# Kernel optimization log

Measured on AMD Instinct MI355X. Metric: run time of the kernel, lower is better.

Reference implementation:

```python
import jax, jax.numpy as jnp
import numpy as np

H = 1024      # hidden_size
NH = 16       # num_heads
HD = H // NH  # head_dim
BETA = 1.0
STEPS = 2
EPS_NORM = 1e-12  # F.normalize eps
EPS_LN = 1e-5     # LayerNorm eps


def setup_inputs() -> dict:
    key = jax.random.key(0)
    ks = jax.random.split(key, 10)
    s = 1.0 / np.sqrt(H)
    return {
        "hidden_states": jax.random.normal(ks[0], (2, 2048, H), jnp.float32),
        "Wq": jax.random.normal(ks[1], (H, H), jnp.float32) * s,
        "bq": jnp.zeros((H,), jnp.float32),
        "Wk": jax.random.normal(ks[2], (H, H), jnp.float32) * s,
        "bk": jnp.zeros((H,), jnp.float32),
        "Wv": jax.random.normal(ks[3], (H, H), jnp.float32) * s,
        "bv": jnp.zeros((H,), jnp.float32),
        "Wo": jax.random.normal(ks[4], (H, H), jnp.float32) * s,
        "bo": jnp.zeros((H,), jnp.float32),
        "ln_w": jnp.ones((H,), jnp.float32),
        "ln_b": jnp.zeros((H,), jnp.float32),
    }


def _l2norm(x):
    n = jnp.linalg.norm(x, axis=-1, keepdims=True)
    return x / jnp.maximum(n, EPS_NORM)


def reference(hidden_states, Wq, bq, Wk, bk, Wv, bv, Wo, bo, ln_w, ln_b):
    B, S, _ = hidden_states.shape
    residual = hidden_states
    # LayerNorm
    mu = jnp.mean(hidden_states, axis=-1, keepdims=True)
    var = jnp.mean(jnp.square(hidden_states - mu), axis=-1, keepdims=True)
    x = (hidden_states - mu) * jax.lax.rsqrt(var + EPS_LN) * ln_w + ln_b
    # projections -> [B,S,NH,HD]
    q = (x @ Wq + bq).reshape(B, S, NH, HD)
    k = (x @ Wk + bk).reshape(B, S, NH, HD)
    v = (x @ Wv + bv).reshape(B, S, NH, HD)
    # cosine-normalized Hopfield retrieval (normalization only once, before loop)
    q = _l2norm(q)
    k = _l2norm(k)
    state = q
    for _ in range(STEPS):
        sim = jnp.einsum('bqhd,bkhd->bqhk', state, k)
        att = jax.nn.softmax(BETA * sim, axis=-1)
        state = jnp.einsum('bqhk,bkhd->bqhd', att, v)
    o = state.reshape(B, S, H) @ Wo + bo
    return residual + o
```

## Files before the change

kernel.cpp:

```cpp
#include <hip/hip_runtime.h>
#include <hip/hip_bf16.h>
#include <math.h>

#define HDIM 1024
#define NHEADS 16
#define HEADD 64
#define SEQLEN 2048
#define NBATCH 2
#define NROWS (NBATCH*SEQLEN)
#define NBH (NBATCH*NHEADS)
#define LOG2E 1.44269504f
#define NT 32

typedef float f32x4 __attribute__((ext_vector_type(4)));
typedef float f32x16 __attribute__((ext_vector_type(16)));
typedef short short8 __attribute__((ext_vector_type(8)));
typedef unsigned short us4v __attribute__((ext_vector_type(4)));

#define GLOBAL_AS __attribute__((address_space(1)))
#define LDS_AS __attribute__((address_space(3)))

union F4 { float4 v; float f[4]; };
union PW { unsigned int u[4]; short8 s; };

static __device__ __forceinline__ unsigned short f2bf(float x) {
    __hip_bfloat16 h = __float2bfloat16(x);
    return *(unsigned short*)&h;
}

__global__ __launch_bounds__(256) void ln_kernel(
        const float* __restrict__ x, const float* __restrict__ w,
        const float* __restrict__ b, unsigned short* __restrict__ xn) {
    int row = blockIdx.x;
    F4 vv; vv.v = ((const float4*)(x + (size_t)row*HDIM))[threadIdx.x];
    float s  = vv.f[0]+vv.f[1]+vv.f[2]+vv.f[3];
    float ss = vv.f[0]*vv.f[0]+vv.f[1]*vv.f[1]+vv.f[2]*vv.f[2]+vv.f[3]*vv.f[3];
    #pragma unroll
    for (int off = 32; off > 0; off >>= 1) {
        s  += __shfl_xor(s, off);
        ss += __shfl_xor(ss, off);
    }
    __shared__ float red[8];
    int wid = threadIdx.x >> 6;
    if ((threadIdx.x & 63) == 0) { red[wid] = s; red[wid+4] = ss; }
    __syncthreads();
    s  = red[0]+red[1]+red[2]+red[3];
    ss = red[4]+red[5]+red[6]+red[7];
    float mean = s * (1.0f/HDIM);
    float var  = ss * (1.0f/HDIM) - mean*mean;
    float rstd = rsqrtf(var + 1e-5f);
    F4 wv; wv.v = ((const float4*)w)[threadIdx.x];
    F4 bv; bv.v = ((const float4*)b)[threadIdx.x];
    us4v o;
    #pragma unroll
    for (int j = 0; j < 4; ++j)
        o[j] = f2bf((vv.f[j]-mean)*rstd*wv.f[j] + bv.f[j]);
    *(us4v*)(xn + (size_t)row*HDIM + threadIdx.x*4) = o;
}

__global__ __launch_bounds__(256) void wconv_kernel(
        const float* __restrict__ W0, const float* __restrict__ W1,
        const float* __restrict__ W2, const float* __restrict__ W3,
        unsigned short* __restrict__ WtBase) {
    __shared__ unsigned short T[64*72];
    int z = blockIdx.z;
    const float* W = (z == 0) ? W0 : (z == 1) ? W1 : (z == 2) ? W2 : W3;
    unsigned short* Wt = WtBase + (size_t)z*HDIM*HDIM;
    int k0 = blockIdx.x*64, n0 = blockIdx.y*64;
    int t = threadIdx.x;
    #pragma unroll
    for (int it = 0; it < 4; ++it) {
        int r = (t>>4) + it*16;
        int c = (t&15)*4;
        F4 x; x.v = *(const float4*)(W + (size_t)(k0+r)*HDIM + n0 + c);
        #pragma unroll
        for (int j = 0; j < 4; ++j) T[(c+j)*72 + r] = f2bf(x.f[j]);
    }
    __syncthreads();
    #pragma unroll
    for (int it = 0; it < 2; ++it) {
        int n = (t>>3) + it*32;
        int ch = t&7;
        short8 rowv = *(const short8*)(T + n*72 + ch*8);
        *(short8*)(Wt + (size_t)(n0+n)*HDIM + k0 + ch*8) = rowv;
    }
}

__global__ __launch_bounds__(256) void gemm_qkv_kernel(
        const unsigned short* __restrict__ A,
        const unsigned short* __restrict__ WtBase,
        const float* __restrict__ bq, const float* __restrict__ bk,
        const float* __restrict__ bv,
        unsigned short* __restrict__ qb, unsigned short* __restrict__ kb,
        unsigned short* __restrict__ vt) {
    __shared__ unsigned short As[2][128*64];
    __shared__ unsigned short Bs[2][128*64];
    int m0 = blockIdx.x * 128;
    int yy = blockIdx.y;
    int mat = yy >> 3;
    int n0 = (yy & 7) * 128;
    const unsigned short* Wt = WtBase + (size_t)mat*HDIM*HDIM;
    const float* bias = (mat == 0) ? bq : (mat == 1) ? bk : bv;
    int t = threadIdx.x;
    int wid = t >> 6, l = t & 63;
    int wm = wid >> 1, wn = wid & 1;
    int lq = l & 15, g = l >> 4;
    f32x4 acc[4][4];
    #pragma unroll
    for (int mi = 0; mi < 4; ++mi)
        #pragma unroll
        for (int ni = 0; ni < 4; ++ni) acc[mi][ni] = 0.0f;

    auto STAGE = [&](int b, int k0) {
        #pragma unroll
        for (int i = 0; i < 4; ++i) {
            int idx = t + 256*i;
            int r = idx >> 3, ch = idx & 7;
            int gch = ch ^ (r & 7);
            __builtin_amdgcn_global_load_lds(
                (const GLOBAL_AS void*)(A + (size_t)(m0+r)*HDIM + k0 + gch*8),
                (LDS_AS void*)((char*)&As[b][0] + idx*16), 16, 0, 0);
            __builtin_amdgcn_global_load_lds(
                (const GLOBAL_AS void*)(Wt + (size_t)(n0+r)*HDIM + k0 + gch*8),
                (LDS_AS void*)((char*)&Bs[b][0] + idx*16), 16, 0, 0);
        }
    };

    STAGE(0, 0);
    asm volatile("s_waitcnt vmcnt(0)" ::: "memory");
    __builtin_amdgcn_s_barrier();
    asm volatile("" ::: "memory");
    int buf = 0;
    for (int ks = 0; ks < 16; ++ks) {
        if (ks < 15) STAGE(buf^1, (ks+1)*64);
        const char* Ab = (const char*)&As[buf][0];
        const char* Bb = (const char*)&Bs[buf][0];
        #pragma unroll
        for (int kc = 0; kc < 2; ++kc) {
            short8 af[4], bf[4];
            #pragma unroll
            for (int mi = 0; mi < 4; ++mi) {
                int r = wm*64 + mi*16 + lq;
                af[mi] = *(const short8*)(Ab + r*128 + (((kc*4+g) ^ (r&7))<<4));
            }
            #pragma unroll
            for (int ni = 0; ni < 4; ++ni) {
                int r = wn*64 + ni*16 + lq;
                bf[ni] = *(const short8*)(Bb + r*128 + (((kc*4+g) ^ (r&7))<<4));
            }
            #pragma unroll
            for (int mi = 0; mi < 4; ++mi)
                #pragma unroll
                for (int ni = 0; ni < 4; ++ni)
                    acc[mi][ni] = __builtin_amdgcn_mfma_f32_16x16x32_bf16(
                        af[mi], bf[ni], acc[mi][ni], 0, 0, 0);
        }
        asm volatile("s_waitcnt vmcnt(0)" ::: "memory");
        __builtin_amdgcn_s_barrier();
        asm volatile("" ::: "memory");
        buf ^= 1;
    }
    float bvv[4];
    #pragma unroll
    for (int ni = 0; ni < 4; ++ni) bvv[ni] = bias[n0 + wn*64 + ni*16 + lq];
    #pragma unroll
    for (int mi = 0; mi < 4; ++mi)
        #pragma unroll
        for (int ni = 0; ni < 4; ++ni)
            #pragma unroll
            for (int i = 0; i < 4; ++i) acc[mi][ni][i] += bvv[ni];
    int h = (n0 >> 6) + wn;
    if (mat <= 1) {
        unsigned short* outp = (mat == 0) ? qb : kb;
        float oscale = (mat == 0) ? LOG2E : 1.0f;
        #pragma unroll
        for (int mi = 0; mi < 4; ++mi) {
            f32x4 ss = 0.0f;
            #pragma unroll
            for (int ni = 0; ni < 4; ++ni)
                #pragma unroll
                for (int i = 0; i < 4; ++i) ss[i] += acc[mi][ni][i]*acc[mi][ni][i];
            #pragma unroll
            for (int off = 1; off < 16; off <<= 1)
                #pragma unroll
                for (int i = 0; i < 4; ++i) ss[i] += __shfl_xor(ss[i], off);
            #pragma unroll
            for (int i = 0; i < 4; ++i) {
                float sc = oscale / fmaxf(sqrtf(ss[i]), 1e-12f);
                int m = m0 + wm*64 + mi*16 + g*4 + i;
                int bb = m >> 11, sq = m & (SEQLEN-1);
                unsigned short* orow = outp
                    + ((size_t)(bb*NHEADS + h)*SEQLEN + sq)*HEADD;
                #pragma unroll
                for (int ni = 0; ni < 4; ++ni)
                    orow[ni*16 + lq] = f2bf(acc[mi][ni][i] * sc);
            }
        }
    } else {
        #pragma unroll
        for (int mi = 0; mi < 4; ++mi) {
            int m = m0 + wm*64 + mi*16 + g*4;
            int bb = m >> 11, sq = m & (SEQLEN-1);
            #pragma unroll
            for (int ni = 0; ni < 4; ++ni) {
                int d = ni*16 + lq;
                us4v pk;
                #pragma unroll
                for (int i = 0; i < 4; ++i) pk[i] = f2bf(acc[mi][ni][i]);
                *(us4v*)(vt + ((size_t)(bb*NHEADS + h)*HEADD + d)*SEQLEN + sq) = pk;
            }
        }
    }
}

__global__ __launch_bounds__(256) void gemm_o_kernel(
        const unsigned short* __restrict__ A,
        const unsigned short* __restrict__ Wt,
        const float* __restrict__ bias,
        const float* __restrict__ residual,
        float* __restrict__ out) {
    __shared__ unsigned short As[2][128*64];
    __shared__ unsigned short Bs[2][64*64];
    int m0 = blockIdx.x * 128;
    int n0 = blockIdx.y * 64;
    int t = threadIdx.x;
    int wid = t >> 6, l = t & 63;
    int wm = wid >> 1, wn = wid & 1;
    int lq = l & 15, g = l >> 4;
    f32x4 acc[4][2];
    #pragma unroll
    for (int mi = 0; mi < 4; ++mi)
        #pragma unroll
        for (int ni = 0; ni < 2; ++ni) acc[mi][ni] = 0.0f;

    auto STAGE = [&](int b, int k0) {
        #pragma unroll
        for (int i = 0; i < 4; ++i) {
            int idx = t + 256*i;
            int r = idx >> 3, ch = idx & 7;
            int gch = ch ^ (r & 7);
            __builtin_amdgcn_global_load_lds(
                (const GLOBAL_AS void*)(A + (size_t)(m0+r)*HDIM + k0 + gch*8),
                (LDS_AS void*)((char*)&As[b][0] + idx*16), 16, 0, 0);
        }
        #pragma unroll
        for (int i = 0; i < 2; ++i) {
            int idx = t + 256*i;
            int r = idx >> 3, ch = idx & 7;
            int gch = ch ^ (r & 7);
            __builtin_amdgcn_global_load_lds(
                (const GLOBAL_AS void*)(Wt + (size_t)(n0+r)*HDIM + k0 + gch*8),
                (LDS_AS void*)((char*)&Bs[b][0] + idx*16), 16, 0, 0);
        }
    };

    STAGE(0, 0);
    asm volatile("s_waitcnt vmcnt(0)" ::: "memory");
    __builtin_amdgcn_s_barrier();
    asm volatile("" ::: "memory");
    int buf = 0;
    for (int ks = 0; ks < 16; ++ks) {
        if (ks < 15) STAGE(buf^1, (ks+1)*64);
        const char* Ab = (const char*)&As[buf][0];
        const char* Bb = (const char*)&Bs[buf][0];
        #pragma unroll
        for (int kc = 0; kc < 2; ++kc) {
            short8 af[4], bf[2];
            #pragma unroll
            for (int mi = 0; mi < 4; ++mi) {
                int r = wm*64 + mi*16 + lq;
                af[mi] = *(const short8*)(Ab + r*128 + (((kc*4+g) ^ (r&7))<<4));
            }
            #pragma unroll
            for (int ni = 0; ni < 2; ++ni) {
                int r = wn*32 + ni*16 + lq;
                bf[ni] = *(const short8*)(Bb + r*128 + (((kc*4+g) ^ (r&7))<<4));
            }
            #pragma unroll
            for (int mi = 0; mi < 4; ++mi)
                #pragma unroll
                for (int ni = 0; ni < 2; ++ni)
                    acc[mi][ni] = __builtin_amdgcn_mfma_f32_16x16x32_bf16(
                        af[mi], bf[ni], acc[mi][ni], 0, 0, 0);
        }
        asm volatile("s_waitcnt vmcnt(0)" ::: "memory");
        __builtin_amdgcn_s_barrier();
        asm volatile("" ::: "memory");
        buf ^= 1;
    }
    float bvv[2];
    #pragma unroll
    for (int ni = 0; ni < 2; ++ni) bvv[ni] = bias[n0 + wn*32 + ni*16 + lq];
    #pragma unroll
    for (int mi = 0; mi < 4; ++mi)
        #pragma unroll
        for (int i = 0; i < 4; ++i) {
            int m = m0 + wm*64 + mi*16 + g*4 + i;
            float* orow = out + (size_t)m*HDIM;
            const float* rrow = residual + (size_t)m*HDIM;
            #pragma unroll
            for (int ni = 0; ni < 2; ++ni) {
                int n = n0 + wn*32 + ni*16 + lq;
                orow[n] = acc[mi][ni][i] + bvv[ni] + rrow[n];
            }
        }
}

__global__ __launch_bounds__(512, 4) void attn_fused_kernel(
        const unsigned short* __restrict__ qg, const unsigned short* __restrict__ kg,
        const unsigned short* __restrict__ vtg, unsigned short* __restrict__ outp) {
    __shared__ char L[4*16384];
    int b = blockIdx.x;
    int bh = (b & 7)*4 + ((b >> 3) & 3);
    int q0 = (b >> 5) * 128;
    int t = threadIdx.x;
    int wid = t >> 6, l = t & 63;
    int wq = wid >> 1, ks = wid & 1;
    int q = l & 31, hi = l >> 5, r7 = q & 7;
    short8 qf[4];
    {
        const unsigned short* qrow = qg + ((size_t)bh*SEQLEN + q0 + wq*32 + q)*HEADD;
        #pragma unroll
        for (int dc = 0; dc < 4; ++dc) qf[dc] = *(const short8*)(qrow + dc*16 + hi*8);
    }
    int koffv[4];
    #pragma unroll
    for (int x = 0; x < 4; ++x) koffv[x] = q*128 + (((x*2 + hi) ^ r7) << 4);
    int vofA = koffv[2*ks], vofB = koffv[2*ks+1];

    f32x16 o0 = 0.0f, o1 = 0.0f;
    float ls = 0.0f;
    const unsigned short* Kg = kg + (size_t)bh*SEQLEN*HEADD;
    const unsigned short* Vg = vtg + (size_t)bh*HEADD*SEQLEN;
    unsigned int* slot = (unsigned int*)(L + wq*4096);
    float* slsum = (float*)(L + 16384 + wq*256);

    int sr = t >> 3, sch = t & 7;
    int sgch = sch ^ (sr & 7);
    const unsigned short* Ksrc = Kg + sr*HEADD + sgch*8;
    const unsigned short* Vsrc = Vg + (size_t)sr*SEQLEN + sgch*8;
    auto STAGE = [&](int buf, int kt) {
        __builtin_amdgcn_global_load_lds(
            (const GLOBAL_AS void*)(Ksrc + (size_t)kt*4096),
            (LDS_AS void*)(L + buf*16384 + t*16), 16, 0, 0);
        __builtin_amdgcn_global_load_lds(
            (const GLOBAL_AS void*)(Vsrc + kt*64),
            (LDS_AS void*)(L + buf*16384 + 8192 + t*16), 16, 0, 0);
    };

    auto doTile = [&](const char* KL, const char* VL) {
        short8 kf0 = *(const short8*)(KL + koffv[0]);
        short8 kf1 = *(const short8*)(KL + koffv[1]);
        short8 kf2 = *(const short8*)(KL + koffv[2]);
        short8 kf3 = *(const short8*)(KL + koffv[3]);
        f32x16 s = 0.0f;
        __builtin_amdgcn_s_setprio(1);
        s = __builtin_amdgcn_mfma_f32_32x32x16_bf16(kf0, qf[0], s, 0, 0, 0);
        s = __builtin_amdgcn_mfma_f32_32x32x16_bf16(kf1, qf[1], s, 0, 0, 0);
        s = __builtin_amdgcn_mfma_f32_32x32x16_bf16(kf2, qf[2], s, 0, 0, 0);
        s = __builtin_amdgcn_mfma_f32_32x32x16_bf16(kf3, qf[3], s, 0, 0, 0);
        __builtin_amdgcn_s_setprio(0);
        unsigned int w[8];
        #pragma unroll
        for (int i = 0; i < 8; ++i) {
            float e0 = __builtin_amdgcn_exp2f(s[2*i]);
            float e1 = __builtin_amdgcn_exp2f(s[2*i+1]);
            ls += e0 + e1;
            asm("v_cvt_pk_bf16_f32 %0, %1, %2" : "=v"(w[i]) : "v"(e0), "v"(e1));
        }
        asm volatile("v_permlane32_swap_b32 %0, %1" : "+v"(w[0]), "+v"(w[2]));
        asm volatile("v_permlane32_swap_b32 %0, %1" : "+v"(w[1]), "+v"(w[3]));
        asm volatile("v_permlane32_swap_b32 %0, %1" : "+v"(w[4]), "+v"(w[6]));
        asm volatile("v_permlane32_swap_b32 %0, %1" : "+v"(w[5]), "+v"(w[7]));
        PW pa, pb;
        pa.u[0]=w[0]; pa.u[1]=w[1]; pa.u[2]=w[2]; pa.u[3]=w[3];
        pb.u[0]=w[4]; pb.u[1]=w[5]; pb.u[2]=w[6]; pb.u[3]=w[7];
        short8 va0 = *(const short8*)(VL + vofA);
        short8 va1 = *(const short8*)(VL + vofA + 4096);
        short8 vb0 = *(const short8*)(VL + vofB);
        short8 vb1 = *(const short8*)(VL + vofB + 4096);
        __builtin_amdgcn_s_setprio(1);
        o0 = __builtin_amdgcn_mfma_f32_32x32x16_bf16(va0, pa.s, o0, 0, 0, 0);
        o1 = __builtin_amdgcn_mfma_f32_32x32x16_bf16(va1, pa.s, o1, 0, 0, 0);
        o0 = __builtin_amdgcn_mfma_f32_32x32x16_bf16(vb0, pb.s, o0, 0, 0, 0);
        o1 = __builtin_amdgcn_mfma_f32_32x32x16_bf16(vb1, pb.s, o1, 0, 0, 0);
        __builtin_amdgcn_s_setprio(0);
    };

    auto runPass = [&]() {
        for (int p = 0; p < NT/2; ++p) {
            int ba = (p & 1) * 2;
            if (p < NT/2 - 1) { STAGE(ba^2, 2*p+2); STAGE((ba^2)+1, 2*p+3); }
            doTile(L + ba*16384 + ks*4096, L + ba*16384 + 8192);
            doTile(L + (ba+1)*16384 + ks*4096, L + (ba+1)*16384 + 8192);
            asm volatile("s_waitcnt vmcnt(0)" ::: "memory");
            __builtin_amdgcn_s_barrier();
            asm volatile("" ::: "memory");
        }
    };

    STAGE(0, 0); STAGE(1, 1);
    asm volatile("s_waitcnt vmcnt(0)" ::: "memory");
    __builtin_amdgcn_s_barrier();
    asm volatile("" ::: "memory");
    runPass();
    ls += __shfl_xor(ls, 32);
    if (ks == 1) {
        #pragma unroll
        for (int i = 0; i < 8; ++i) {
            unsigned int u;
            asm("v_cvt_pk_bf16_f32 %0, %1, %2" : "=v"(u) : "v"(o0[2*i]), "v"(o0[2*i+1]));
            slot[i*64 + l] = u;
            asm("v_cvt_pk_bf16_f32 %0, %1, %2" : "=v"(u) : "v"(o1[2*i]), "v"(o1[2*i+1]));
            slot[(8+i)*64 + l] = u;
        }
        slsum[l] = ls;
        asm volatile("s_waitcnt lgkmcnt(0)" ::: "memory");
    }
    __builtin_amdgcn_s_barrier();
    asm volatile("" ::: "memory");
    if (ks == 0) {
        #pragma unroll
        for (int i = 0; i < 8; ++i) {
            unsigned int u = slot[i*64 + l];
            o0[2*i]   += __uint_as_float(u << 16);
            o0[2*i+1] += __uint_as_float(u & 0xffff0000u);
            u = slot[(8+i)*64 + l];
            o1[2*i]   += __uint_as_float(u << 16);
            o1[2*i+1] += __uint_as_float(u & 0xffff0000u);
        }
        float osc = LOG2E / (ls + slsum[l]);
        unsigned int w0[8], w1[8];
        #pragma unroll
        for (int i = 0; i < 8; ++i) {
            float a0 = o0[2*i]*osc, a1 = o0[2*i+1]*osc;
            asm("v_cvt_pk_bf16_f32 %0, %1, %2" : "=v"(w0[i]) : "v"(a0), "v"(a1));
            float b0 = o1[2*i]*osc, b1 = o1[2*i+1]*osc;
            asm("v_cvt_pk_bf16_f32 %0, %1, %2" : "=v"(w1[i]) : "v"(b0), "v"(b1));
        }
        asm volatile("v_permlane32_swap_b32 %0, %1" : "+v"(w0[0]), "+v"(w0[2]));
        asm volatile("v_permlane32_swap_b32 %0, %1" : "+v"(w0[1]), "+v"(w0[3]));
        asm volatile("v_permlane32_swap_b32 %0, %1" : "+v"(w0[4]), "+v"(w0[6]));
        asm volatile("v_permlane32_swap_b32 %0, %1" : "+v"(w0[5]), "+v"(w0[7]));
        asm volatile("v_permlane32_swap_b32 %0, %1" : "+v"(w1[0]), "+v"(w1[2]));
        asm volatile("v_permlane32_swap_b32 %0, %1" : "+v"(w1[1]), "+v"(w1[3]));
        asm volatile("v_permlane32_swap_b32 %0, %1" : "+v"(w1[4]), "+v"(w1[6]));
        asm volatile("v_permlane32_swap_b32 %0, %1" : "+v"(w1[5]), "+v"(w1[7]));
        PW pa;
        pa.u[0]=w0[0]; pa.u[1]=w0[1]; pa.u[2]=w0[2]; pa.u[3]=w0[3]; qf[0]=pa.s;
        pa.u[0]=w0[4]; pa.u[1]=w0[5]; pa.u[2]=w0[6]; pa.u[3]=w0[7]; qf[1]=pa.s;
        pa.u[0]=w1[0]; pa.u[1]=w1[1]; pa.u[2]=w1[2]; pa.u[3]=w1[3]; qf[2]=pa.s;
        pa.u[0]=w1[4]; pa.u[1]=w1[5]; pa.u[2]=w1[6]; pa.u[3]=w1[7]; qf[3]=pa.s;
        #pragma unroll
        for (int i = 0; i < 8; ++i) {
            slot[i*64 + l] = w0[i];
            slot[(8+i)*64 + l] = w1[i];
        }
        asm volatile("s_waitcnt lgkmcnt(0)" ::: "memory");
    }
    __builtin_amdgcn_s_barrier();
    asm volatile("" ::: "memory");
    if (ks == 1) {
        PW pa;
        pa.u[0]=slot[0*64+l]; pa.u[1]=slot[1*64+l]; pa.u[2]=slot[2*64+l]; pa.u[3]=slot[3*64+l]; qf[0]=pa.s;
        pa.u[0]=slot[4*64+l]; pa.u[1]=slot[5*64+l]; pa.u[2]=slot[6*64+l]; pa.u[3]=slot[7*64+l]; qf[1]=pa.s;
        pa.u[0]=slot[8*64+l]; pa.u[1]=slot[9*64+l]; pa.u[2]=slot[10*64+l]; pa.u[3]=slot[11*64+l]; qf[2]=pa.s;
        pa.u[0]=slot[12*64+l]; pa.u[1]=slot[13*64+l]; pa.u[2]=slot[14*64+l]; pa.u[3]=slot[15*64+l]; qf[3]=pa.s;
    }
    asm volatile("s_waitcnt lgkmcnt(0)" ::: "memory");
    __builtin_amdgcn_s_barrier();
    asm volatile("" ::: "memory");
    o0 = 0.0f; o1 = 0.0f; ls = 0.0f;
    STAGE(0, 0); STAGE(1, 1);
    asm volatile("s_waitcnt vmcnt(0)" ::: "memory");
    __builtin_amdgcn_s_barrier();
    asm volatile("" ::: "memory");
    runPass();
    ls += __shfl_xor(ls, 32);
    if (ks == 1) {
        #pragma unroll
        for (int i = 0; i < 8; ++i) {
            unsigned int u;
            asm("v_cvt_pk_bf16_f32 %0, %1, %2" : "=v"(u) : "v"(o0[2*i]), "v"(o0[2*i+1]));
            slot[i*64 + l] = u;
            asm("v_cvt_pk_bf16_f32 %0, %1, %2" : "=v"(u) : "v"(o1[2*i]), "v"(o1[2*i+1]));
            slot[(8+i)*64 + l] = u;
        }
        slsum[l] = ls;
        asm volatile("s_waitcnt lgkmcnt(0)" ::: "memory");
    }
    __builtin_amdgcn_s_barrier();
    asm volatile("" ::: "memory");
    if (ks == 0) {
        #pragma unroll
        for (int i = 0; i < 8; ++i) {
            unsigned int u = slot[i*64 + l];
            o0[2*i]   += __uint_as_float(u << 16);
            o0[2*i+1] += __uint_as_float(u & 0xffff0000u);
            u = slot[(8+i)*64 + l];
            o1[2*i]   += __uint_as_float(u << 16);
            o1[2*i+1] += __uint_as_float(u & 0xffff0000u);
        }
        float osc = 1.0f / (ls + slsum[l]);
        int bb = bh >> 4, hh = bh & 15;
        unsigned short* orow = outp + ((size_t)bb*SEQLEN + q0 + wq*32 + q)*HDIM + hh*HEADD;
        const int dtab[8] = {0,2,8,10,16,18,24,26};
        #pragma unroll
        for (int i = 0; i < 8; ++i) {
            int d = dtab[i] + 4*hi;
            unsigned int wv;
            float a0 = o0[2*i]*osc, a1 = o0[2*i+1]*osc;
            asm("v_cvt_pk_bf16_f32 %0, %1, %2" : "=v"(wv) : "v"(a0), "v"(a1));
            *(unsigned int*)(orow + d) = wv;
            float c0 = o1[2*i]*osc, c1 = o1[2*i+1]*osc;
            asm("v_cvt_pk_bf16_f32 %0, %1, %2" : "=v"(wv) : "v"(c0), "v"(c1));
            *(unsigned int*)(orow + 32 + d) = wv;
        }
    }
}

extern "C" void kernel_launch(void* const* d_in, const int* in_sizes, int n_in,
                              void* d_out, int out_size, void* d_ws, size_t ws_size,
                              hipStream_t stream) {
    const float* hs = (const float*)d_in[0];
    const float* Wq = (const float*)d_in[1];
    const float* bq = (const float*)d_in[2];
    const float* Wk = (const float*)d_in[3];
    const float* bk = (const float*)d_in[4];
    const float* Wv = (const float*)d_in[5];
    const float* bv = (const float*)d_in[6];
    const float* Wo = (const float*)d_in[7];
    const float* bo = (const float*)d_in[8];
    const float* lw = (const float*)d_in[9];
    const float* lb = (const float*)d_in[10];
    unsigned short* ws16 = (unsigned short*)d_ws;
    const size_t NE = (size_t)NROWS * HDIM;
    const size_t WE = (size_t)HDIM * HDIM;
    unsigned short* xn  = ws16;
    unsigned short* Wtq = xn + NE;
    unsigned short* Wto = Wtq + 3*WE;
    unsigned short* qb  = Wtq + 4*WE;
    unsigned short* kb  = qb + NE;
    unsigned short* vt  = kb + NE;
    unsigned short* s2  = vt + NE;

    ln_kernel<<<NROWS, 256, 0, stream>>>(hs, lw, lb, xn);
    wconv_kernel<<<dim3(HDIM/64, HDIM/64, 4), 256, 0, stream>>>(Wq, Wk, Wv, Wo, Wtq);
    gemm_qkv_kernel<<<dim3(NROWS/128, 24), 256, 0, stream>>>(xn, Wtq, bq, bk, bv, qb, kb, vt);
    attn_fused_kernel<<<NBH*16, 512, 0, stream>>>(qb, kb, vt, s2);
    gemm_o_kernel<<<dim3(NROWS/128, HDIM/64), 256, 0, stream>>>(s2, Wto, bo, hs, (float*)d_out);
}
```

Before: 168.7 us.

## Switch attention K/V staging to a 3-buffer ring with per-tile partial waits

Replaces the pair-wise double buffering of 64-key tiles (four 16KB LDS buffers) with a triple-buffered ring (three buffers). It prefetches two tiles ahead, processes one tile per iteration, and waits with vmcnt(2) so the newest prefetch stays in flight across the barrier. The V fragment loads are hoisted to just after the QK MFMAs, with sched_barriers pinning the order. The aim is to overlap global loads with compute more continuously and to use less LDS, which may allow more blocks per CU. The cost is twice as many barriers per pass and ordering constraints that depend on exact vmcnt accounting.

Result: faster. 160.1 us (-5.1%).

```diff
diff --git a/kernel.cpp b/kernel.cpp
--- a/kernel.cpp
+++ b/kernel.cpp
@@ -309,7 +309,7 @@
 __global__ __launch_bounds__(512, 4) void attn_fused_kernel(
         const unsigned short* __restrict__ qg, const unsigned short* __restrict__ kg,
         const unsigned short* __restrict__ vtg, unsigned short* __restrict__ outp) {
-    __shared__ char L[4*16384];
+    __shared__ char L[3*16384];
     int b = blockIdx.x;
     int bh = (b & 7)*4 + ((b >> 3) & 3);
     int q0 = (b >> 5) * 128;
@@ -323,10 +323,12 @@
         #pragma unroll
         for (int dc = 0; dc < 4; ++dc) qf[dc] = *(const short8*)(qrow + dc*16 + hi*8);
     }
-    int koffv[4];
-    #pragma unroll
-    for (int x = 0; x < 4; ++x) koffv[x] = q*128 + (((x*2 + hi) ^ r7) << 4);
-    int vofA = koffv[2*ks], vofB = koffv[2*ks+1];
+    int koffK0 = q*128 + (((0 + hi) ^ r7) << 4) + ks*4096;
+    int koffK1 = q*128 + (((2 + hi) ^ r7) << 4) + ks*4096;
+    int koffK2 = q*128 + (((4 + hi) ^ r7) << 4) + ks*4096;
+    int koffK3 = q*128 + (((6 + hi) ^ r7) << 4) + ks*4096;
+    int vofA = q*128 + (((4*ks + hi) ^ r7) << 4);
+    int vofB = q*128 + (((4*ks + 2 + hi) ^ r7) << 4);
 
     f32x16 o0 = 0.0f, o1 = 0.0f;
     float ls = 0.0f;
@@ -348,61 +350,75 @@
             (LDS_AS void*)(L + buf*16384 + 8192 + t*16), 16, 0, 0);
     };
 
-    auto doTile = [&](const char* KL, const char* VL) {
-        short8 kf0 = *(const short8*)(KL + koffv[0]);
-        short8 kf1 = *(const short8*)(KL + koffv[1]);
-        short8 kf2 = *(const short8*)(KL + koffv[2]);
-        short8 kf3 = *(const short8*)(KL + koffv[3]);
+    auto doTile = [&](const char* T) {
+        short8 k0 = *(const short8*)(T + koffK0);
+        short8 k1 = *(const short8*)(T + koffK1);
+        short8 k2 = *(const short8*)(T + koffK2);
+        short8 k3 = *(const short8*)(T + koffK3);
         f32x16 s = 0.0f;
-        __builtin_amdgcn_s_setprio(1);
-        s = __builtin_amdgcn_mfma_f32_32x32x16_bf16(kf0, qf[0], s, 0, 0, 0);
-        s = __builtin_amdgcn_mfma_f32_32x32x16_bf16(kf1, qf[1], s, 0, 0, 0);
-        s = __builtin_amdgcn_mfma_f32_32x32x16_bf16(kf2, qf[2], s, 0, 0, 0);
-        s = __builtin_amdgcn_mfma_f32_32x32x16_bf16(kf3, qf[3], s, 0, 0, 0);
-        __builtin_amdgcn_s_setprio(0);
+        s = __builtin_amdgcn_mfma_f32_32x32x16_bf16(k0, qf[0], s, 0, 0, 0);
+        s = __builtin_amdgcn_mfma_f32_32x32x16_bf16(k1, qf[1], s, 0, 0, 0);
+        s = __builtin_amdgcn_mfma_f32_32x32x16_bf16(k2, qf[2], s, 0, 0, 0);
+        s = __builtin_amdgcn_mfma_f32_32x32x16_bf16(k3, qf[3], s, 0, 0, 0);
+        __builtin_amdgcn_sched_barrier(0);
+        short8 va0 = *(const short8*)(T + 8192 + vofA);
+        short8 va1 = *(const short8*)(T + 8192 + vofA + 4096);
+        short8 vb0 = *(const short8*)(T + 8192 + vofB);
+        short8 vb1 = *(const short8*)(T + 8192 + vofB + 4096);
         unsigned int w[8];
+        float p = 0.0f;
         #pragma unroll
         for (int i = 0; i < 8; ++i) {
             float e0 = __builtin_amdgcn_exp2f(s[2*i]);
             float e1 = __builtin_amdgcn_exp2f(s[2*i+1]);
-            ls += e0 + e1;
+            p += e0 + e1;
             asm("v_cvt_pk_bf16_f32 %0, %1, %2" : "=v"(w[i]) : "v"(e0), "v"(e1));
         }
-        asm volatile("v_permlane32_swap_b32 %0, %1" : "+v"(w[0]), "+v"(w[2]));
-        asm volatile("v_permlane32_swap_b32 %0, %1" : "+v"(w[1]), "+v"(w[3]));
-        asm volatile("v_permlane32_swap_b32 %0, %1" : "+v"(w[4]), "+v"(w[6]));
-        asm volatile("v_permlane32_swap_b32 %0, %1" : "+v"(w[5]), "+v"(w[7]));
-        PW pa, pb;
-        pa.u[0]=w[0]; pa.u[1]=w[1]; pa.u[2]=w[2]; pa.u[3]=w[3];
-        pb.u[0]=w[4]; pb.u[1]=w[5]; pb.u[2]=w[6]; pb.u[3]=w[7];
-        short8 va0 = *(const short8*)(VL + vofA);
-        short8 va1 = *(const short8*)(VL + vofA + 4096);
-        short8 vb0 = *(const short8*)(VL + vofB);
-        short8 vb1 = *(const short8*)(VL + vofB + 4096);
-        __builtin_amdgcn_s_setprio(1);
-        o0 = __builtin_amdgcn_mfma_f32_32x32x16_bf16(va0, pa.s, o0, 0, 0, 0);
-        o1 = __builtin_amdgcn_mfma_f32_32x32x16_bf16(va1, pa.s, o1, 0, 0, 0);
-        o0 = __builtin_amdgcn_mfma_f32_32x32x16_bf16(vb0, pb.s, o0, 0, 0, 0);
-        o1 = __builtin_amdgcn_mfma_f32_32x32x16_bf16(vb1, pb.s, o1, 0, 0, 0);
-        __builtin_amdgcn_s_setprio(0);
+        ls += p;
+        asm("v_permlane32_swap_b32 %0, %1" : "+v"(w[0]), "+v"(w[2]));
+        asm("v_permlane32_swap_b32 %0, %1" : "+v"(w[1]), "+v"(w[3]));
+        asm("v_permlane32_swap_b32 %0, %1" : "+v"(w[4]), "+v"(w[6]));
+        asm("v_permlane32_swap_b32 %0, %1" : "+v"(w[5]), "+v"(w[7]));
+        __builtin_amdgcn_sched_barrier(0);
+        {
+            PW pa, pb;
+            pa.u[0]=w[0]; pa.u[1]=w[1]; pa.u[2]=w[2]; pa.u[3]=w[3];
+            pb.u[0]=w[4]; pb.u[1]=w[5]; pb.u[2]=w[6]; pb.u[3]=w[7];
+            __builtin_amdgcn_s_setprio(1);
+            o0 = __builtin_amdgcn_mfma_f32_32x32x16_bf16(va0, pa.s, o0, 0, 0, 0);
+            o1 = __builtin_amdgcn_mfma_f32_32x32x16_bf16(va1, pa.s, o1, 0, 0, 0);
+            o0 = __builtin_amdgcn_mfma_f32_32x32x16_bf16(vb0, pb.s, o0, 0, 0, 0);
+            o1 = __builtin_amdgcn_mfma_f32_32x32x16_bf16(vb1, pb.s, o1, 0, 0, 0);
+            __builtin_amdgcn_s_setprio(0);
+        }
     };
 
     auto runPass = [&]() {
-        for (int p = 0; p < NT/2; ++p) {
-            int ba = (p & 1) * 2;
-            if (p < NT/2 - 1) { STAGE(ba^2, 2*p+2); STAGE((ba^2)+1, 2*p+3); }
-            doTile(L + ba*16384 + ks*4096, L + ba*16384 + 8192);
-            doTile(L + (ba+1)*16384 + ks*4096, L + (ba+1)*16384 + 8192);
-            asm volatile("s_waitcnt vmcnt(0)" ::: "memory");
+        int cur = 0;
+        #pragma unroll 1
+        for (int kt = 0; kt < NT; ++kt) {
+            bool pre = (kt + 2 < NT);
+            if (pre) {
+                int nb = cur + 2; if (nb >= 3) nb -= 3;
+                STAGE(nb, kt + 2);
+            }
+            doTile(L + cur*16384);
+            if (pre) asm volatile("s_waitcnt vmcnt(2)" ::: "memory");
+            else     asm volatile("s_waitcnt vmcnt(0)" ::: "memory");
             __builtin_amdgcn_s_barrier();
             asm volatile("" ::: "memory");
+            cur = (cur == 2) ? 0 : cur + 1;
         }
     };
 
-    STAGE(0, 0); STAGE(1, 1);
-    asm volatile("s_waitcnt vmcnt(0)" ::: "memory");
-    __builtin_amdgcn_s_barrier();
-    asm volatile("" ::: "memory");
+    auto prologue = [&]() {
+        STAGE(0, 0); STAGE(1, 1);
+        asm volatile("s_waitcnt vmcnt(2)" ::: "memory");
+        __builtin_amdgcn_s_barrier();
+        asm volatile("" ::: "memory");
+    };
+
+    prologue();
     runPass();
     ls += __shfl_xor(ls, 32);
     if (ks == 1) {
@@ -471,10 +487,7 @@
     __builtin_amdgcn_s_barrier();
     asm volatile("" ::: "memory");
     o0 = 0.0f; o1 = 0.0f; ls = 0.0f;
-    STAGE(0, 0); STAGE(1, 1);
-    asm volatile("s_waitcnt vmcnt(0)" ::: "memory");
-    __builtin_amdgcn_s_barrier();
-    asm volatile("" ::: "memory");
+    prologue();
     runPass();
     ls += __shfl_xor(ls, 32);
     if (ks == 1) {
```
